# Kernel optimization log

Measured on AMD Instinct MI355X. Metric: run time of the kernel, lower is better.

The kernel has to match this reference:

```python
import jax, jax.numpy as jnp
import numpy as np

B, C, H, W = 4, 256, 64, 64
OUT_C = 256
K = 3          # kernel_size
P = K // 2     # zero padding
EPS = 1e-5     # F.layer_norm default eps


def setup_inputs() -> dict:
    key = jax.random.key(0)
    ks = jax.random.split(key, 9)
    s = 0.02
    return {
        "x":  jax.random.normal(ks[0], (B, C, H, W), dtype=jnp.float32),
        "Wq": jax.random.normal(ks[1], (C, C), dtype=jnp.float32) * s,
        "bq": jax.random.normal(ks[2], (C,), dtype=jnp.float32) * s,
        "Wk": jax.random.normal(ks[3], (C, C), dtype=jnp.float32) * s,
        "bk": jax.random.normal(ks[4], (C,), dtype=jnp.float32) * s,
        "Wv": jax.random.normal(ks[5], (C, C), dtype=jnp.float32) * s,
        "bv": jax.random.normal(ks[6], (C,), dtype=jnp.float32) * s,
        "Wo": jax.random.normal(ks[7], (OUT_C, C), dtype=jnp.float32) * s,
        "bo": jax.random.normal(ks[8], (OUT_C,), dtype=jnp.float32) * s,
    }


def _forward(x, Wq, bq, Wk, bk, Wv, bv, Wo, bo):
    # LayerNorm over the last two dims [H, W], no affine (per (b, c) plane).
    mu = jnp.mean(x, axis=(2, 3), keepdims=True)
    var = jnp.var(x, axis=(2, 3), keepdims=True)
    xn = (x - mu) * jax.lax.rsqrt(var + EPS)

    xh = jnp.transpose(xn, (0, 2, 3, 1))            # [B, H, W, C]
    scale = jnp.asarray(C, xh.dtype) ** -0.5        # depth_scale = C**-0.5

    # Query only at each center pixel (only the center output is kept).
    q = (xh @ Wq.T + bq) * scale                    # [B, H, W, C]

    # Zero-pad the normalized input, then project: padded positions get K=bk, V=bv
    # exactly as torch's Linear applied to zero-padded windows.
    xp = jnp.pad(xh, ((0, 0), (P, P), (P, P), (0, 0)))  # [B, H+2P, W+2P, C]
    Kp = xp @ Wk.T + bk
    Vp = xp @ Wv.T + bv

    # Gather the K*K neighborhood for every pixel (small fixed loop over 9 shifts).
    Kw = jnp.stack([Kp[:, i:i + H, j:j + W, :] for i in range(K) for j in range(K)], axis=3)  # [B,H,W,9,C]
    Vw = jnp.stack([Vp[:, i:i + H, j:j + W, :] for i in range(K) for j in range(K)], axis=3)  # [B,H,W,9,C]

    logits = jnp.einsum('bhwc,bhwnc->bhwn', q, Kw)  # [B, H, W, 9]
    attn = jax.nn.softmax(logits, axis=-1)
    ctx = jnp.einsum('bhwn,bhwnc->bhwc', attn, Vw)  # [B, H, W, C]

    out = ctx @ Wo.T + bo                           # [B, H, W, OUT_C]
    return jnp.transpose(out, (0, 3, 1, 2))         # [B, OUT_C, H, W]


def reference(x, Wq, bq, Wk, bk, Wv, bv, Wo, bo):
    return _forward(x, Wq, bq, Wk, bk, Wv, bv, Wo, bo)
```

## Files before the change

kernel.cpp:

```cpp
#include <hip/hip_runtime.h>

typedef unsigned short u16;
typedef unsigned int   u32;

typedef __attribute__((ext_vector_type(4))) float f32x4;
typedef __attribute__((ext_vector_type(8))) short bf16x8;

#define HWDIM 4096
#define CDIM  256

__device__ __forceinline__ float bf2f(u16 u) { return __uint_as_float(((u32)u) << 16); }
__device__ __forceinline__ u16 f2bf(float f) {
    u32 u = __float_as_uint(f);
    u32 r = (u + 0x7fffu + ((u >> 16) & 1u)) >> 16;
    return (u16)r;
}

#define GLL16(g, l) \
    __builtin_amdgcn_global_load_lds((const __attribute__((address_space(1))) u32*)(g), \
                                     (__attribute__((address_space(3))) u32*)(l), 16, 0, 0)

__global__ __launch_bounds__(256) void fill_kernel(float* __restrict__ out, int n) {
    int i = blockIdx.x * 256 + threadIdx.x;
    if (i < n) out[i] = 1.0f;
}

__global__ __launch_bounds__(256) void prep_kernel(const float* __restrict__ x,
                                                   const float* __restrict__ Wq,
                                                   const float* __restrict__ Wk,
                                                   const float* __restrict__ Wv,
                                                   const float* __restrict__ Wo,
                                                   const float* __restrict__ bq,
                                                   const float* __restrict__ bk,
                                                   const float* __restrict__ bv,
                                                   u16* __restrict__ Wqkv,
                                                   u16* __restrict__ Woc,
                                                   float* __restrict__ biasStack,
                                                   float2* __restrict__ stats) {
    int bx = blockIdx.x;
    int t = threadIdx.x;
    if (bx < 1024) {
        const float* px = x + (size_t)bx * HWDIM;
        float sum = 0.f, ss = 0.f;
#pragma unroll
        for (int it = 0; it < 4; ++it) {
            float4 v = *(const float4*)(px + (t + it * 256) * 4);
            sum += v.x + v.y + v.z + v.w;
            ss  += v.x * v.x + v.y * v.y + v.z * v.z + v.w * v.w;
        }
#pragma unroll
        for (int o = 32; o; o >>= 1) { sum += __shfl_xor(sum, o); ss += __shfl_xor(ss, o); }
        __shared__ float s1[4], s2[4];
        int wid = t >> 6, lane = t & 63;
        if (lane == 0) { s1[wid] = sum; s2[wid] = ss; }
        __syncthreads();
        if (t == 0) {
            float S = s1[0] + s1[1] + s1[2] + s1[3];
            float Q = s2[0] + s2[1] + s2[2] + s2[3];
            float mu  = S * (1.f / HWDIM);
            float var = Q * (1.f / HWDIM) - mu * mu;
            stats[bx] = make_float2(mu, rsqrtf(var + 1e-5f));
        }
        return;
    }
    int idx = bx - 1024;
    int yy = idx >> 6, xx = idx & 63;
    if (yy == 4) {
        if (xx == 0) {
            biasStack[t]       = bq[t] * 0.0625f;
            biasStack[t + 256] = bk[t];
            biasStack[t + 512] = bv[t];
        }
        return;
    }
    const float* s; u16* d; float sc = 1.f;
    if (yy == 0)      { s = Wq; d = Wqkv;          sc = 0.0625f; }
    else if (yy == 1) { s = Wk; d = Wqkv + 65536; }
    else if (yy == 2) { s = Wv; d = Wqkv + 131072; }
    else              { s = Wo; d = Woc; }
    int i = (xx * 256 + t) * 4;
    float4 f = *(const float4*)(s + i);
    u16 tmp[4] = {f2bf(f.x * sc), f2bf(f.y * sc), f2bf(f.z * sc), f2bf(f.w * sc)};
    *(uint2*)(d + i) = *(uint2*)tmp;
}

__global__ __launch_bounds__(256) void ln_transpose_kernel(const float* __restrict__ x,
                                                           const float2* __restrict__ stats,
                                                           u16* __restrict__ xh) {
    __shared__ __align__(16) u16 tile[64 * 72];
    int b  = blockIdx.z;
    int c0 = blockIdx.y * 64;
    int p0 = blockIdx.x * 64;
    int t  = threadIdx.x;
    int c_loc = t >> 2;
    int pc    = (t & 3) * 16;
    int plane = b * CDIM + c0 + c_loc;
    float2 st = stats[plane];
    const float* px = x + (size_t)plane * HWDIM + p0 + pc;
#pragma unroll
    for (int j2 = 0; j2 < 4; j2++) {
        float4 v = *(const float4*)(px + j2 * 4);
        int p = pc + j2 * 4;
        tile[(p + 0) * 72 + c_loc] = f2bf((v.x - st.x) * st.y);
        tile[(p + 1) * 72 + c_loc] = f2bf((v.y - st.x) * st.y);
        tile[(p + 2) * 72 + c_loc] = f2bf((v.z - st.x) * st.y);
        tile[(p + 3) * 72 + c_loc] = f2bf((v.w - st.x) * st.y);
    }
    __syncthreads();
    int cc = (t & 7) * 8;
#pragma unroll
    for (int it = 0; it < 2; ++it) {
        int p_loc = (t >> 3) + it * 32;
        uint4 val = *(uint4*)&tile[p_loc * 72 + cc];
        *(uint4*)(xh + ((size_t)(b * HWDIM + p0 + p_loc)) * CDIM + c0 + cc) = val;
    }
}

__global__ __launch_bounds__(256) void gemm_qkv_kernel(const u16* __restrict__ xh,
                                                       const u16* __restrict__ Wqkv,
                                                       const float* __restrict__ biasStack,
                                                       u16* __restrict__ qkv) {
    __shared__ __align__(16) u16 lA[128 * 32];
    __shared__ __align__(16) u16 lB[128 * 32];
    int t = threadIdx.x, lane = t & 63, wid = t >> 6;
    int waveM = wid >> 1, waveN = wid & 1;
    int m0 = blockIdx.x * 128;
    int n0 = blockIdx.y * 128;
    f32x4 acc[4][4];
#pragma unroll
    for (int i = 0; i < 4; i++)
#pragma unroll
        for (int j = 0; j < 4; j++) acc[i][j] = (f32x4){0.f, 0.f, 0.f, 0.f};
    int fr = lane & 15, kq = (lane >> 4) * 8;
    int r = t >> 2, kc = (t & 3) * 8;
    const u16* gA0 = xh + (size_t)(m0 + r) * 256 + kc;
    const u16* gA1 = gA0 + 64 * 256;
    const u16* gB0 = Wqkv + (size_t)(n0 + r) * 256 + kc;
    const u16* gB1 = gB0 + 64 * 256;
    u16* lA0 = lA + wid * 512;
    u16* lA1 = lA0 + 2048;
    u16* lB0 = lB + wid * 512;
    u16* lB1 = lB0 + 2048;
    for (int k0 = 0; k0 < 256; k0 += 32) {
        GLL16(gA0 + k0, lA0);
        GLL16(gA1 + k0, lA1);
        GLL16(gB0 + k0, lB0);
        GLL16(gB1 + k0, lB1);
        __syncthreads();
        bf16x8 af[4], bfr[4];
#pragma unroll
        for (int i = 0; i < 4; i++) af[i]  = *(const bf16x8*)&lA[(waveM * 64 + i * 16 + fr) * 32 + kq];
#pragma unroll
        for (int j = 0; j < 4; j++) bfr[j] = *(const bf16x8*)&lB[(waveN * 64 + j * 16 + fr) * 32 + kq];
#pragma unroll
        for (int i = 0; i < 4; i++)
#pragma unroll
            for (int j = 0; j < 4; j++)
                acc[i][j] = __builtin_amdgcn_mfma_f32_16x16x32_bf16(af[i], bfr[j], acc[i][j], 0, 0, 0);
        __syncthreads();
    }
    int r0 = (lane >> 4) * 4;
#pragma unroll
    for (int j = 0; j < 4; j++) {
        int ng = n0 + waveN * 64 + j * 16 + fr;
        float bval = biasStack[ng];
#pragma unroll
        for (int i = 0; i < 4; i++) {
            int mrow = m0 + waveM * 64 + i * 16 + r0;
#pragma unroll
            for (int rr = 0; rr < 4; rr++)
                qkv[(size_t)(mrow + rr) * 768 + ng] = f2bf(acc[i][j][rr] + bval);
        }
    }
}

__global__ __launch_bounds__(256) void attn_kernel(const u16* __restrict__ qkv,
                                                   const float* __restrict__ biasStack,
                                                   u16* __restrict__ ctx) {
    int t = threadIdx.x, wid = t >> 6, lane = t & 63;
    int pix = blockIdx.x * 4 + wid;
    int h = (pix >> 6) & 63, w = pix & 63;
    int c4 = lane << 2;
    const u16* row = qkv + (size_t)pix * 768;
    uint2 qr = *(const uint2*)(row + c4);
    float q0 = __uint_as_float(qr.x << 16), q1 = __uint_as_float(qr.x & 0xffff0000u);
    float q2 = __uint_as_float(qr.y << 16), q3 = __uint_as_float(qr.y & 0xffff0000u);
    float4 kbias = *(const float4*)(biasStack + 256 + c4);
    float4 vbias = *(const float4*)(biasStack + 512 + c4);
    float part[9];
    int off[9];
#pragma unroll
    for (int n = 0; n < 9; n++) {
        int dy = n / 3 - 1, dx = n % 3 - 1;
        int hh = h + dy, ww = w + dx;
        bool inb = ((unsigned)hh < 64u) && ((unsigned)ww < 64u);
        off[n] = inb ? ((pix + dy * 64 + dx) * 768) : -1;
        float k0, k1, k2, k3;
        if (off[n] >= 0) {
            uint2 kr = *(const uint2*)(qkv + off[n] + 256 + c4);
            k0 = __uint_as_float(kr.x << 16); k1 = __uint_as_float(kr.x & 0xffff0000u);
            k2 = __uint_as_float(kr.y << 16); k3 = __uint_as_float(kr.y & 0xffff0000u);
        } else {
            k0 = kbias.x; k1 = kbias.y; k2 = kbias.z; k3 = kbias.w;
        }
        part[n] = q0 * k0 + q1 * k1 + q2 * k2 + q3 * k3;
    }
#pragma unroll
    for (int o = 32; o; o >>= 1) {
#pragma unroll
        for (int n = 0; n < 9; n++) part[n] += __shfl_xor(part[n], o);
    }
    float m = part[0];
#pragma unroll
    for (int n = 1; n < 9; n++) m = fmaxf(m, part[n]);
    float e[9], s = 0.f;
#pragma unroll
    for (int n = 0; n < 9; n++) { e[n] = __expf(part[n] - m); s += e[n]; }
    float inv = 1.f / s;
    float a0 = 0.f, a1 = 0.f, a2 = 0.f, a3 = 0.f;
#pragma unroll
    for (int n = 0; n < 9; n++) {
        float v0, v1, v2, v3;
        if (off[n] >= 0) {
            uint2 vr = *(const uint2*)(qkv + off[n] + 512 + c4);
            v0 = __uint_as_float(vr.x << 16); v1 = __uint_as_float(vr.x & 0xffff0000u);
            v2 = __uint_as_float(vr.y << 16); v3 = __uint_as_float(vr.y & 0xffff0000u);
        } else {
            v0 = vbias.x; v1 = vbias.y; v2 = vbias.z; v3 = vbias.w;
        }
        float wn = e[n] * inv;
        a0 += wn * v0; a1 += wn * v1; a2 += wn * v2; a3 += wn * v3;
    }
    u32 lo = (u32)f2bf(a0) | ((u32)f2bf(a1) << 16);
    u32 hi = (u32)f2bf(a2) | ((u32)f2bf(a3) << 16);
    *(uint2*)(ctx + (size_t)pix * 256 + c4) = make_uint2(lo, hi);
}

__global__ __launch_bounds__(256) void gemm_out_kernel(const u16* __restrict__ ctx,
                                                       const u16* __restrict__ Wo,
                                                       const float* __restrict__ bo,
                                                       float* __restrict__ out) {
    __shared__ __align__(16) u16 lA[128 * 32];
    __shared__ __align__(16) u16 lB[64 * 32];
    int t = threadIdx.x, lane = t & 63, wid = t >> 6;
    int waveM = wid >> 1, waveN = wid & 1;
    int m0 = blockIdx.x * 128;
    int n0 = blockIdx.y * 64;
    f32x4 acc[4][2];
#pragma unroll
    for (int i = 0; i < 4; i++)
#pragma unroll
        for (int j = 0; j < 2; j++) acc[i][j] = (f32x4){0.f, 0.f, 0.f, 0.f};
    int fr = lane & 15, kq = (lane >> 4) * 8;
    int r = t >> 2, kc = (t & 3) * 8;
    const u16* gA0 = ctx + (size_t)(m0 + r) * 256 + kc;
    const u16* gA1 = gA0 + 64 * 256;
    const u16* gB0 = Wo + (size_t)(n0 + r) * 256 + kc;
    u16* lA0 = lA + wid * 512;
    u16* lA1 = lA0 + 2048;
    u16* lB0 = lB + wid * 512;
    for (int k0 = 0; k0 < 256; k0 += 32) {
        GLL16(gA0 + k0, lA0);
        GLL16(gA1 + k0, lA1);
        GLL16(gB0 + k0, lB0);
        __syncthreads();
        bf16x8 af[4], bfr[2];
#pragma unroll
        for (int i = 0; i < 4; i++) af[i]  = *(const bf16x8*)&lA[(waveM * 64 + i * 16 + fr) * 32 + kq];
#pragma unroll
        for (int j = 0; j < 2; j++) bfr[j] = *(const bf16x8*)&lB[(waveN * 32 + j * 16 + fr) * 32 + kq];
#pragma unroll
        for (int i = 0; i < 4; i++)
#pragma unroll
            for (int j = 0; j < 2; j++)
                acc[i][j] = __builtin_amdgcn_mfma_f32_16x16x32_bf16(af[i], bfr[j], acc[i][j], 0, 0, 0);
        __syncthreads();
    }
    int r0 = (lane >> 4) * 4;
#pragma unroll
    for (int j = 0; j < 2; j++) {
        int ng = n0 + waveN * 32 + j * 16 + fr;
        float bval = bo[ng];
#pragma unroll
        for (int i = 0; i < 4; i++) {
            int m = m0 + waveM * 64 + i * 16 + r0;
            int bidx = m >> 12;
            int p = m & 4095;
            float4 vv = make_float4(acc[i][j][0] + bval, acc[i][j][1] + bval,
                                    acc[i][j][2] + bval, acc[i][j][3] + bval);
            *(float4*)(out + ((size_t)(bidx * 256 + ng)) * HWDIM + p) = vv;
        }
    }
}

extern "C" void kernel_launch(void* const* d_in, const int* in_sizes, int n_in,
                              void* d_out, int out_size, void* d_ws, size_t ws_size,
                              hipStream_t stream) {
    const float* x  = (const float*)d_in[0];
    const float* Wq = (const float*)d_in[1];
    const float* bq = (const float*)d_in[2];
    const float* Wk = (const float*)d_in[3];
    const float* bk = (const float*)d_in[4];
    const float* Wv = (const float*)d_in[5];
    const float* bv = (const float*)d_in[6];
    const float* Wo = (const float*)d_in[7];
    const float* bo = (const float*)d_in[8];
    float* out = (float*)d_out;

    char* wsb = (char*)d_ws;
    const size_t MB = 1ull << 20;

    if (ws_size < 34 * MB) {
        hipLaunchKernelGGL(fill_kernel, dim3((out_size + 255) / 256), dim3(256), 0, stream,
                           out, out_size);
        return;
    }

    float2* stats     = (float2*)wsb;
    float*  biasStack = (float*)(wsb + 16 * 1024);
    u16* Wqkv = (u16*)(wsb + 64 * 1024);
    u16* Woc  = (u16*)(wsb + 448 * 1024);
    u16* xh   = (u16*)(wsb + 1 * MB);
    u16* qkv  = (u16*)(wsb + 9 * MB);
    u16* ctx  = xh;

    hipLaunchKernelGGL(prep_kernel, dim3(1344), dim3(256), 0, stream,
                       x, Wq, Wk, Wv, Wo, bq, bk, bv, Wqkv, Woc, biasStack, stats);
    hipLaunchKernelGGL(ln_transpose_kernel, dim3(64, 4, 4), dim3(256), 0, stream, x, stats, xh);
    hipLaunchKernelGGL(gemm_qkv_kernel,     dim3(128, 6),   dim3(256), 0, stream,
                       xh, Wqkv, biasStack, qkv);
    hipLaunchKernelGGL(attn_kernel,         dim3(4096),     dim3(256), 0, stream,
                       qkv, biasStack, ctx);
    hipLaunchKernelGGL(gemm_out_kernel,     dim3(128, 4),   dim3(256), 0, stream,
                       ctx, Woc, bo, out);
}
```

Measured before the change: 129.9 us.

## Fuse neighborhood attention with output projection and regroup prep kernels

The attention step now writes its bf16 context for 32 pixels into shared memory, and the same block runs the output-projection GEMM against the full Wo. This removes the ctx round trip through global memory and one kernel launch. The prep work is also regrouped: LN stats get their own kernel, and the LN-transpose is merged with the weight conversion. The risk is that each attention block reloads all of Wo (128 KB) from L2, and the GEMM tile is small (32 rows), so MFMA reuse drops.

```diff
diff --git a/kernel.cpp b/kernel.cpp
--- a/kernel.cpp
+++ b/kernel.cpp
@@ -25,41 +25,74 @@
     if (i < n) out[i] = 1.0f;
 }
 
-__global__ __launch_bounds__(256) void prep_kernel(const float* __restrict__ x,
-                                                   const float* __restrict__ Wq,
-                                                   const float* __restrict__ Wk,
-                                                   const float* __restrict__ Wv,
-                                                   const float* __restrict__ Wo,
-                                                   const float* __restrict__ bq,
-                                                   const float* __restrict__ bk,
-                                                   const float* __restrict__ bv,
-                                                   u16* __restrict__ Wqkv,
-                                                   u16* __restrict__ Woc,
-                                                   float* __restrict__ biasStack,
-                                                   float2* __restrict__ stats) {
+__global__ __launch_bounds__(256) void ln_stats_kernel(const float* __restrict__ x,
+                                                       float2* __restrict__ stats) {
+    int plane = blockIdx.x;
+    int t = threadIdx.x;
+    const float* px = x + (size_t)plane * HWDIM;
+    float sum = 0.f, ss = 0.f;
+#pragma unroll
+    for (int it = 0; it < 4; ++it) {
+        float4 v = *(const float4*)(px + (t + it * 256) * 4);
+        sum += v.x + v.y + v.z + v.w;
+        ss  += v.x * v.x + v.y * v.y + v.z * v.z + v.w * v.w;
+    }
+#pragma unroll
+    for (int o = 32; o; o >>= 1) { sum += __shfl_xor(sum, o); ss += __shfl_xor(ss, o); }
+    __shared__ float s1[4], s2[4];
+    int wid = t >> 6, lane = t & 63;
+    if (lane == 0) { s1[wid] = sum; s2[wid] = ss; }
+    __syncthreads();
+    if (t == 0) {
+        float S = s1[0] + s1[1] + s1[2] + s1[3];
+        float Q = s2[0] + s2[1] + s2[2] + s2[3];
+        float mu  = S * (1.f / HWDIM);
+        float var = Q * (1.f / HWDIM) - mu * mu;
+        stats[plane] = make_float2(mu, rsqrtf(var + 1e-5f));
+    }
+}
+
+__global__ __launch_bounds__(256) void trans_wconv_kernel(const float* __restrict__ x,
+                                                          const float2* __restrict__ stats,
+                                                          const float* __restrict__ Wq,
+                                                          const float* __restrict__ Wk,
+                                                          const float* __restrict__ Wv,
+                                                          const float* __restrict__ Wo,
+                                                          const float* __restrict__ bq,
+                                                          const float* __restrict__ bk,
+                                                          const float* __restrict__ bv,
+                                                          u16* __restrict__ xh,
+                                                          u16* __restrict__ Wqkv,
+                                                          u16* __restrict__ Woc,
+                                                          float* __restrict__ biasStack) {
+    __shared__ __align__(16) u16 tile[64 * 72];
     int bx = blockIdx.x;
-    int t = threadIdx.x;
+    int t  = threadIdx.x;
     if (bx < 1024) {
-        const float* px = x + (size_t)bx * HWDIM;
-        float sum = 0.f, ss = 0.f;
-#pragma unroll
-        for (int it = 0; it < 4; ++it) {
-            float4 v = *(const float4*)(px + (t + it * 256) * 4);
-            sum += v.x + v.y + v.z + v.w;
-            ss  += v.x * v.x + v.y * v.y + v.z * v.z + v.w * v.w;
-        }
-#pragma unroll
-        for (int o = 32; o; o >>= 1) { sum += __shfl_xor(sum, o); ss += __shfl_xor(ss, o); }
-        __shared__ float s1[4], s2[4];
-        int wid = t >> 6, lane = t & 63;
-        if (lane == 0) { s1[wid] = sum; s2[wid] = ss; }
-        __syncthreads();
-        if (t == 0) {
-            float S = s1[0] + s1[1] + s1[2] + s1[3];
-            float Q = s2[0] + s2[1] + s2[2] + s2[3];
-            float mu  = S * (1.f / HWDIM);
-            float var = Q * (1.f / HWDIM) - mu * mu;
-            stats[bx] = make_float2(mu, rsqrtf(var + 1e-5f));
+        int b  = bx >> 8;
+        int c0 = ((bx >> 6) & 3) * 64;
+        int p0 = (bx & 63) * 64;
+        int c_loc = t >> 2;
+        int pc    = (t & 3) * 16;
+        int plane = b * CDIM + c0 + c_loc;
+        float2 st = stats[plane];
+        const float* px = x + (size_t)plane * HWDIM + p0 + pc;
+#pragma unroll
+        for (int j2 = 0; j2 < 4; j2++) {
+            float4 v = *(const float4*)(px + j2 * 4);
+            int p = pc + j2 * 4;
+            tile[(p + 0) * 72 + c_loc] = f2bf((v.x - st.x) * st.y);
+            tile[(p + 1) * 72 + c_loc] = f2bf((v.y - st.x) * st.y);
+            tile[(p + 2) * 72 + c_loc] = f2bf((v.z - st.x) * st.y);
+            tile[(p + 3) * 72 + c_loc] = f2bf((v.w - st.x) * st.y);
+        }
+        __syncthreads();
+        int cc = (t & 7) * 8;
+#pragma unroll
+        for (int it = 0; it < 2; ++it) {
+            int p_loc = (t >> 3) + it * 32;
+            uint4 val = *(uint4*)&tile[p_loc * 72 + cc];
+            *(uint4*)(xh + ((size_t)(b * HWDIM + p0 + p_loc)) * CDIM + c0 + cc) = val;
         }
         return;
     }
@@ -82,38 +115,6 @@
     float4 f = *(const float4*)(s + i);
     u16 tmp[4] = {f2bf(f.x * sc), f2bf(f.y * sc), f2bf(f.z * sc), f2bf(f.w * sc)};
     *(uint2*)(d + i) = *(uint2*)tmp;
-}
-
-__global__ __launch_bounds__(256) void ln_transpose_kernel(const float* __restrict__ x,
-                                                           const float2* __restrict__ stats,
-                                                           u16* __restrict__ xh) {
-    __shared__ __align__(16) u16 tile[64 * 72];
-    int b  = blockIdx.z;
-    int c0 = blockIdx.y * 64;
-    int p0 = blockIdx.x * 64;
-    int t  = threadIdx.x;
-    int c_loc = t >> 2;
-    int pc    = (t & 3) * 16;
-    int plane = b * CDIM + c0 + c_loc;
-    float2 st = stats[plane];
-    const float* px = x + (size_t)plane * HWDIM + p0 + pc;
-#pragma unroll
-    for (int j2 = 0; j2 < 4; j2++) {
-        float4 v = *(const float4*)(px + j2 * 4);
-        int p = pc + j2 * 4;
-        tile[(p + 0) * 72 + c_loc] = f2bf((v.x - st.x) * st.y);
-        tile[(p + 1) * 72 + c_loc] = f2bf((v.y - st.x) * st.y);
-        tile[(p + 2) * 72 + c_loc] = f2bf((v.z - st.x) * st.y);
-        tile[(p + 3) * 72 + c_loc] = f2bf((v.w - st.x) * st.y);
-    }
-    __syncthreads();
-    int cc = (t & 7) * 8;
-#pragma unroll
-    for (int it = 0; it < 2; ++it) {
-        int p_loc = (t >> 3) + it * 32;
-        uint4 val = *(uint4*)&tile[p_loc * 72 + cc];
-        *(uint4*)(xh + ((size_t)(b * HWDIM + p0 + p_loc)) * CDIM + c0 + cc) = val;
-    }
 }
 
 __global__ __launch_bounds__(256) void gemm_qkv_kernel(const u16* __restrict__ xh,
@@ -174,122 +175,110 @@
     }
 }
 
-__global__ __launch_bounds__(256) void attn_kernel(const u16* __restrict__ qkv,
-                                                   const float* __restrict__ biasStack,
-                                                   u16* __restrict__ ctx) {
-    int t = threadIdx.x, wid = t >> 6, lane = t & 63;
-    int pix = blockIdx.x * 4 + wid;
-    int h = (pix >> 6) & 63, w = pix & 63;
-    int c4 = lane << 2;
-    const u16* row = qkv + (size_t)pix * 768;
-    uint2 qr = *(const uint2*)(row + c4);
-    float q0 = __uint_as_float(qr.x << 16), q1 = __uint_as_float(qr.x & 0xffff0000u);
-    float q2 = __uint_as_float(qr.y << 16), q3 = __uint_as_float(qr.y & 0xffff0000u);
-    float4 kbias = *(const float4*)(biasStack + 256 + c4);
-    float4 vbias = *(const float4*)(biasStack + 512 + c4);
-    float part[9];
-    int off[9];
-#pragma unroll
-    for (int n = 0; n < 9; n++) {
-        int dy = n / 3 - 1, dx = n % 3 - 1;
-        int hh = h + dy, ww = w + dx;
-        bool inb = ((unsigned)hh < 64u) && ((unsigned)ww < 64u);
-        off[n] = inb ? ((pix + dy * 64 + dx) * 768) : -1;
-        float k0, k1, k2, k3;
-        if (off[n] >= 0) {
-            uint2 kr = *(const uint2*)(qkv + off[n] + 256 + c4);
-            k0 = __uint_as_float(kr.x << 16); k1 = __uint_as_float(kr.x & 0xffff0000u);
-            k2 = __uint_as_float(kr.y << 16); k3 = __uint_as_float(kr.y & 0xffff0000u);
-        } else {
-            k0 = kbias.x; k1 = kbias.y; k2 = kbias.z; k3 = kbias.w;
-        }
-        part[n] = q0 * k0 + q1 * k1 + q2 * k2 + q3 * k3;
-    }
-#pragma unroll
-    for (int o = 32; o; o >>= 1) {
-#pragma unroll
-        for (int n = 0; n < 9; n++) part[n] += __shfl_xor(part[n], o);
-    }
-    float m = part[0];
-#pragma unroll
-    for (int n = 1; n < 9; n++) m = fmaxf(m, part[n]);
-    float e[9], s = 0.f;
-#pragma unroll
-    for (int n = 0; n < 9; n++) { e[n] = __expf(part[n] - m); s += e[n]; }
-    float inv = 1.f / s;
-    float a0 = 0.f, a1 = 0.f, a2 = 0.f, a3 = 0.f;
-#pragma unroll
-    for (int n = 0; n < 9; n++) {
-        float v0, v1, v2, v3;
-        if (off[n] >= 0) {
-            uint2 vr = *(const uint2*)(qkv + off[n] + 512 + c4);
-            v0 = __uint_as_float(vr.x << 16); v1 = __uint_as_float(vr.x & 0xffff0000u);
-            v2 = __uint_as_float(vr.y << 16); v3 = __uint_as_float(vr.y & 0xffff0000u);
-        } else {
-            v0 = vbias.x; v1 = vbias.y; v2 = vbias.z; v3 = vbias.w;
-        }
-        float wn = e[n] * inv;
-        a0 += wn * v0; a1 += wn * v1; a2 += wn * v2; a3 += wn * v3;
-    }
-    u32 lo = (u32)f2bf(a0) | ((u32)f2bf(a1) << 16);
-    u32 hi = (u32)f2bf(a2) | ((u32)f2bf(a3) << 16);
-    *(uint2*)(ctx + (size_t)pix * 256 + c4) = make_uint2(lo, hi);
-}
-
-__global__ __launch_bounds__(256) void gemm_out_kernel(const u16* __restrict__ ctx,
+#define ASTR 264
+__global__ __launch_bounds__(256) void attn_out_kernel(const u16* __restrict__ qkv,
+                                                       const float* __restrict__ biasStack,
                                                        const u16* __restrict__ Wo,
                                                        const float* __restrict__ bo,
                                                        float* __restrict__ out) {
-    __shared__ __align__(16) u16 lA[128 * 32];
-    __shared__ __align__(16) u16 lB[64 * 32];
-    int t = threadIdx.x, lane = t & 63, wid = t >> 6;
+    __shared__ __align__(16) u16 lA[32 * ASTR];
+    __shared__ __align__(16) u16 lB[256 * 32];
+    int t = threadIdx.x, wid = t >> 6, lane = t & 63;
+    int pix0 = blockIdx.x * 32;
+    int c4 = lane << 2;
+    const float4 kbias = *(const float4*)(biasStack + 256 + c4);
+    const float4 vbias = *(const float4*)(biasStack + 512 + c4);
+    for (int it = 0; it < 8; ++it) {
+        int pl = wid * 8 + it;
+        int pix = pix0 + pl;
+        int h = (pix >> 6) & 63, w = pix & 63;
+        const u16* row = qkv + (size_t)pix * 768;
+        uint2 qr = *(const uint2*)(row + c4);
+        float q0 = __uint_as_float(qr.x << 16), q1 = __uint_as_float(qr.x & 0xffff0000u);
+        float q2 = __uint_as_float(qr.y << 16), q3 = __uint_as_float(qr.y & 0xffff0000u);
+        float part[9];
+        int off[9];
+#pragma unroll
+        for (int n = 0; n < 9; n++) {
+            int dy = n / 3 - 1, dx = n % 3 - 1;
+            int hh = h + dy, ww = w + dx;
+            bool inb = ((unsigned)hh < 64u) && ((unsigned)ww < 64u);
+            off[n] = inb ? ((pix + dy * 64 + dx) * 768) : -1;
+            float k0, k1, k2, k3;
+            if (off[n] >= 0) {
+                uint2 kr = *(const uint2*)(qkv + off[n] + 256 + c4);
+                k0 = __uint_as_float(kr.x << 16); k1 = __uint_as_float(kr.x & 0xffff0000u);
+                k2 = __uint_as_float(kr.y << 16); k3 = __uint_as_float(kr.y & 0xffff0000u);
+            } else {
+                k0 = kbias.x; k1 = kbias.y; k2 = kbias.z; k3 = kbias.w;
+            }
+            part[n] = q0 * k0 + q1 * k1 + q2 * k2 + q3 * k3;
+        }
+#pragma unroll
+        for (int o = 32; o; o >>= 1) {
+#pragma unroll
+            for (int n = 0; n < 9; n++) part[n] += __shfl_xor(part[n], o);
+        }
+        float m = part[0];
+#pragma unroll
+        for (int n = 1; n < 9; n++) m = fmaxf(m, part[n]);
+        float e[9], s = 0.f;
+#pragma unroll
+        for (int n = 0; n < 9; n++) { e[n] = __expf(part[n] - m); s += e[n]; }
+        float inv = 1.f / s;
+        float a0 = 0.f, a1 = 0.f, a2 = 0.f, a3 = 0.f;
+#pragma unroll
+        for (int n = 0; n < 9; n++) {
+            float v0, v1, v2, v3;
+            if (off[n] >= 0) {
+                uint2 vr = *(const uint2*)(qkv + off[n] + 512 + c4);
+                v0 = __uint_as_float(vr.x << 16); v1 = __uint_as_float(vr.x & 0xffff0000u);
+                v2 = __uint_as_float(vr.y << 16); v3 = __uint_as_float(vr.y & 0xffff0000u);
+            } else {
+                v0 = vbias.x; v1 = vbias.y; v2 = vbias.z; v3 = vbias.w;
+            }
+            float wn = e[n] * inv;
+            a0 += wn * v0; a1 += wn * v1; a2 += wn * v2; a3 += wn * v3;
+        }
+        u32 lo = (u32)f2bf(a0) | ((u32)f2bf(a1) << 16);
+        u32 hi = (u32)f2bf(a2) | ((u32)f2bf(a3) << 16);
+        *(uint2*)&lA[pl * ASTR + c4] = make_uint2(lo, hi);
+    }
+    __syncthreads();
     int waveM = wid >> 1, waveN = wid & 1;
-    int m0 = blockIdx.x * 128;
-    int n0 = blockIdx.y * 64;
-    f32x4 acc[4][2];
-#pragma unroll
-    for (int i = 0; i < 4; i++)
-#pragma unroll
-        for (int j = 0; j < 2; j++) acc[i][j] = (f32x4){0.f, 0.f, 0.f, 0.f};
     int fr = lane & 15, kq = (lane >> 4) * 8;
+    f32x4 acc[8];
+#pragma unroll
+    for (int j = 0; j < 8; j++) acc[j] = (f32x4){0.f, 0.f, 0.f, 0.f};
     int r = t >> 2, kc = (t & 3) * 8;
-    const u16* gA0 = ctx + (size_t)(m0 + r) * 256 + kc;
-    const u16* gA1 = gA0 + 64 * 256;
-    const u16* gB0 = Wo + (size_t)(n0 + r) * 256 + kc;
-    u16* lA0 = lA + wid * 512;
-    u16* lA1 = lA0 + 2048;
+    const u16* gB = Wo + (size_t)r * 256 + kc;
     u16* lB0 = lB + wid * 512;
     for (int k0 = 0; k0 < 256; k0 += 32) {
-        GLL16(gA0 + k0, lA0);
-        GLL16(gA1 + k0, lA1);
-        GLL16(gB0 + k0, lB0);
-        __syncthreads();
-        bf16x8 af[4], bfr[2];
-#pragma unroll
-        for (int i = 0; i < 4; i++) af[i]  = *(const bf16x8*)&lA[(waveM * 64 + i * 16 + fr) * 32 + kq];
-#pragma unroll
-        for (int j = 0; j < 2; j++) bfr[j] = *(const bf16x8*)&lB[(waveN * 32 + j * 16 + fr) * 32 + kq];
-#pragma unroll
-        for (int i = 0; i < 4; i++)
-#pragma unroll
-            for (int j = 0; j < 2; j++)
-                acc[i][j] = __builtin_amdgcn_mfma_f32_16x16x32_bf16(af[i], bfr[j], acc[i][j], 0, 0, 0);
+        GLL16(gB + k0,             lB0);
+        GLL16(gB + k0 +  64 * 256, lB0 + 2048);
+        GLL16(gB + k0 + 128 * 256, lB0 + 4096);
+        GLL16(gB + k0 + 192 * 256, lB0 + 6144);
+        __syncthreads();
+        bf16x8 af = *(const bf16x8*)&lA[(waveM * 16 + fr) * ASTR + k0 + kq];
+#pragma unroll
+        for (int j = 0; j < 8; j++) {
+            bf16x8 bfr = *(const bf16x8*)&lB[(waveN * 128 + j * 16 + fr) * 32 + kq];
+            acc[j] = __builtin_amdgcn_mfma_f32_16x16x32_bf16(af, bfr, acc[j], 0, 0, 0);
+        }
         __syncthreads();
     }
     int r0 = (lane >> 4) * 4;
 #pragma unroll
-    for (int j = 0; j < 2; j++) {
-        int ng = n0 + waveN * 32 + j * 16 + fr;
+    for (int j = 0; j < 8; j++) {
+        int ng = waveN * 128 + j * 16 + fr;
         float bval = bo[ng];
-#pragma unroll
-        for (int i = 0; i < 4; i++) {
-            int m = m0 + waveM * 64 + i * 16 + r0;
-            int bidx = m >> 12;
-            int p = m & 4095;
-            float4 vv = make_float4(acc[i][j][0] + bval, acc[i][j][1] + bval,
-                                    acc[i][j][2] + bval, acc[i][j][3] + bval);
-            *(float4*)(out + ((size_t)(bidx * 256 + ng)) * HWDIM + p) = vv;
-        }
+        int m_loc = waveM * 16 + r0;
+        int pix = pix0 + m_loc;
+        int bidx = pix >> 12;
+        int p = pix & 4095;
+        float4 vv = make_float4(acc[j][0] + bval, acc[j][1] + bval,
+                                acc[j][2] + bval, acc[j][3] + bval);
+        *(float4*)(out + ((size_t)(bidx * 256 + ng)) * HWDIM + p) = vv;
     }
 }
 
@@ -322,15 +311,12 @@
     u16* Woc  = (u16*)(wsb + 448 * 1024);
     u16* xh   = (u16*)(wsb + 1 * MB);
     u16* qkv  = (u16*)(wsb + 9 * MB);
-    u16* ctx  = xh;
-
-    hipLaunchKernelGGL(prep_kernel, dim3(1344), dim3(256), 0, stream,
-                       x, Wq, Wk, Wv, Wo, bq, bk, bv, Wqkv, Woc, biasStack, stats);
-    hipLaunchKernelGGL(ln_transpose_kernel, dim3(64, 4, 4), dim3(256), 0, stream, x, stats, xh);
-    hipLaunchKernelGGL(gemm_qkv_kernel,     dim3(128, 6),   dim3(256), 0, stream,
+
+    hipLaunchKernelGGL(ln_stats_kernel,   dim3(1024), dim3(256), 0, stream, x, stats);
+    hipLaunchKernelGGL(trans_wconv_kernel, dim3(1344), dim3(256), 0, stream,
+                       x, stats, Wq, Wk, Wv, Wo, bq, bk, bv, xh, Wqkv, Woc, biasStack);
+    hipLaunchKernelGGL(gemm_qkv_kernel,   dim3(128, 6), dim3(256), 0, stream,
                        xh, Wqkv, biasStack, qkv);
-    hipLaunchKernelGGL(attn_kernel,         dim3(4096),     dim3(256), 0, stream,
-                       qkv, biasStack, ctx);
-    hipLaunchKernelGGL(gemm_out_kernel,     dim3(128, 4),   dim3(256), 0, stream,
-                       ctx, Woc, bo, out);
-}
+    hipLaunchKernelGGL(attn_out_kernel,   dim3(512),  dim3(256), 0, stream,
+                       qkv, biasStack, Woc, bo, out);
+}
```

After: 157.6 us. 21.3% more time.
